# Kernel tuning notes

Measured on AMD Instinct MI355X. Metric: run time of the kernel, lower is better.

The kernel has to match this reference:

```python
import jax, jax.numpy as jnp
import numpy as np

K = 5  # box-blur width along disparity axis

def _blur_disparity(x):
    # depthwise conv1d with ones(K)/K kernel, zero 'same' padding, along axis 1
    N, D, H, W = x.shape
    xp = jnp.pad(x, ((0, 0), (K // 2, K // 2), (0, 0), (0, 0)))
    acc = xp[:, 0:D]
    for s in range(1, K):
        acc = acc + xp[:, s:s + D]
    return acc / K

def _modal_mask(x):
    N, D, H, W = x.shape
    index = jnp.argmax(x, axis=1, keepdims=True)                 # [N,1,H,W] int
    d = jnp.arange(D, dtype=x.dtype).reshape(1, D, 1, 1)
    d2 = jnp.arange(D + 1, dtype=x.dtype).reshape(1, D + 1, 1, 1)
    ones = jnp.ones((N, 1, H, W), dtype=x.dtype)
    x_diff_r = jnp.diff(x, axis=1, prepend=ones, append=ones)    # [N,D+1,H,W]
    x_diff_l = jnp.diff(x, axis=1, prepend=ones)                 # [N,D,H,W]
    # right edge of dominant mode: first positive diff strictly right of peak
    ind_r = ((x_diff_r * (d2 > index)) > 0).astype(jnp.int32)
    index_r = jnp.argmax(ind_r, axis=1, keepdims=True) - 1
    # left edge: last negative diff at/left of peak
    ind_l = ((x_diff_l * (d <= index)) < 0).astype(jnp.int32)
    index_l = D - 1 - jnp.argmax(jnp.flip(ind_l, axis=1), axis=1, keepdims=True)
    mask1 = (d >= index_l) & (d <= index_r)
    r = jnp.minimum(index_r - index, index - index_l)
    mask2 = (d >= index - r) & (d <= index + r)
    valid = jnp.abs(2 * index - index_r - index_l) < 3           # near-symmetric mode
    return jnp.where(valid, mask1, mask2)                        # bool [N,D,H,W]

def setup_inputs() -> dict:
    key = jax.random.key(0)
    N, D, H, W = 2, 192, 256, 512
    x = jax.random.uniform(key, (N, D, H, W), dtype=jnp.float32)
    return {"x": x}

def reference(x) -> jnp.ndarray:
    N, D, H, W = x.shape
    disp = jnp.arange(D, dtype=x.dtype).reshape(1, D, 1, 1)
    x_blur = _blur_disparity(x)
    mask = _modal_mask(x_blur)
    y = x * mask                       # primary mode mass
    z = x - y
    x_blur2 = x_blur * (~mask)
    z = z * _modal_mask(x_blur2)       # secondary mode mass
    valid = (jnp.sum(y, axis=1) >= jnp.sum(z, axis=1)).astype(jnp.float32)[:, None]
    xm = valid * y + (1.0 - valid) * z
    xm = xm / jnp.sum(xm, axis=1, keepdims=True)
    out = jnp.sum(xm * disp, axis=1, keepdims=True)  # [N,1,H,W]
    return out
```

## Files before the change

### kernel.cpp

```cpp
#include <hip/hip_runtime.h>
#include <math.h>

namespace {
constexpr int D     = 192;
constexpr int HW    = 256 * 512;
constexpr int TOTAL = 2 * HW;

__device__ __forceinline__ float div5(float s) {
    const float c = 0.2f;
    float q = s * c;
    float r = __builtin_fmaf(-5.0f, q, s);
    return __builtin_fmaf(r, c, q);
}

struct Machine {
    float bprev, maxv;
    int   index, last_fall, index_l, index_r;
    bool  r_found;

    __device__ __forceinline__ void init() {
        bprev = 1.0f;
        maxv  = -INFINITY;
        index = 0; last_fall = 0; index_l = 0;
        index_r = D - 1;
        r_found = false;
    }

    __device__ __forceinline__ void step(int d, float b) {
        float diff = b - bprev;
        bool fall  = diff < 0.0f;
        last_fall  = fall ? d : last_fall;
        bool am    = b > maxv;
        maxv       = am ? b : maxv;
        index      = am ? d : index;
        index_l    = am ? last_fall : index_l;
        bool rise  = (diff > 0.0f) & (!r_found) & (!am);
        index_r    = am ? (D - 1) : (rise ? (d - 1) : index_r);
        r_found    = am ? false : (r_found | rise);
        bprev      = b;
    }

    __device__ __forceinline__ void finish(int& lo, int& hi) const {
        int r = min(index_r - index, index - index_l);
        int t = 2 * index - index_r - index_l;
        bool valid = (t > -3) && (t < 3);
        lo = valid ? index_l : (index - r);
        hi = valid ? index_r : (index + r);
    }
};

__device__ __forceinline__ bool in_range(int d, int lo, unsigned width) {
    return (unsigned)(d - lo) <= width;
}
}

extern "C" __global__ void __launch_bounds__(256)
dme_kernel(const float* __restrict__ x, float* __restrict__ out)
{
    const int n  = blockIdx.x >> 9;
    const int hw = ((blockIdx.x & 511) << 8) | threadIdx.x;
    const float* __restrict__ col = x + (size_t)n * (size_t)(D * HW) + hw;

    Machine m1; m1.init();
    {
        float w0 = 0.f, w1 = 0.f;
        float w2 = col[0], w3 = col[HW];
        float cur[8], nxt[8];
        #pragma unroll
        for (int j = 0; j < 8; ++j) cur[j] = col[(size_t)(2 + j) * HW];
        int d = 0;
        auto step8 = [&](const float (&L)[8]) {
            #pragma unroll
            for (int j = 0; j < 8; ++j) {
                float s = w0 + w1; s += w2; s += w3; s += L[j];
                m1.step(d, div5(s));
                w0 = w1; w1 = w2; w2 = w3; w3 = L[j]; ++d;
            }
        };
        for (int k = 0; k < 22; ++k) {
            #pragma unroll
            for (int j = 0; j < 8; ++j) nxt[j] = col[(size_t)(8 * k + 10 + j) * HW];
            step8(cur);
            #pragma unroll
            for (int j = 0; j < 8; ++j) cur[j] = nxt[j];
        }
        #pragma unroll
        for (int j = 0; j < 8; ++j)
            nxt[j] = (186 + j < D) ? col[(size_t)(186 + j) * HW] : 0.0f;
        step8(cur);
        #pragma unroll
        for (int j = 0; j < 8; ++j) cur[j] = nxt[j];
        step8(cur);
    }
    int lo1, hi1; m1.finish(lo1, hi1);
    unsigned wd1 = (unsigned)(hi1 - lo1);

    Machine m2; m2.init();
    float sum_y = 0.f, wsum_y = 0.f;
    {
        float w0 = 0.f, w1 = 0.f;
        float w2 = col[0], w3 = col[HW];
        float cur[8], nxt[8];
        #pragma unroll
        for (int j = 0; j < 8; ++j) cur[j] = col[(size_t)(2 + j) * HW];
        int d = 0; float fd = 0.0f;
        auto step8 = [&](const float (&L)[8]) {
            #pragma unroll
            for (int j = 0; j < 8; ++j) {
                float s = w0 + w1; s += w2; s += w3; s += L[j];
                float b = div5(s);
                bool in1 = in_range(d, lo1, wd1);
                m2.step(d, in1 ? 0.0f : b);
                sum_y += in1 ? w2 : 0.f;
                float t = in1 ? fd : 0.f;
                wsum_y = __builtin_fmaf(t, w2, wsum_y);
                w0 = w1; w1 = w2; w2 = w3; w3 = L[j]; ++d; fd += 1.0f;
            }
        };
        for (int k = 0; k < 22; ++k) {
            #pragma unroll
            for (int j = 0; j < 8; ++j) nxt[j] = col[(size_t)(8 * k + 10 + j) * HW];
            step8(cur);
            #pragma unroll
            for (int j = 0; j < 8; ++j) cur[j] = nxt[j];
        }
        #pragma unroll
        for (int j = 0; j < 8; ++j)
            nxt[j] = (186 + j < D) ? col[(size_t)(186 + j) * HW] : 0.0f;
        step8(cur);
        #pragma unroll
        for (int j = 0; j < 8; ++j) cur[j] = nxt[j];
        step8(cur);
    }
    int lo2, hi2; m2.finish(lo2, hi2);
    unsigned wd2 = (unsigned)(hi2 - lo2);

    float sum_z = 0.f, wsum_z = 0.f;
    {
        float cur[8], nxt[8];
        #pragma unroll
        for (int j = 0; j < 8; ++j) cur[j] = col[(size_t)j * HW];
        int d = 0; float fd = 0.0f;
        auto step8 = [&](const float (&L)[8]) {
            #pragma unroll
            for (int j = 0; j < 8; ++j) {
                bool z = in_range(d, lo2, wd2) & !in_range(d, lo1, wd1);
                sum_z += z ? L[j] : 0.f;
                float t = z ? fd : 0.f;
                wsum_z = __builtin_fmaf(t, L[j], wsum_z);
                ++d; fd += 1.0f;
            }
        };
        for (int k = 0; k < 23; ++k) {
            #pragma unroll
            for (int j = 0; j < 8; ++j) nxt[j] = col[(size_t)(8 * k + 8 + j) * HW];
            step8(cur);
            #pragma unroll
            for (int j = 0; j < 8; ++j) cur[j] = nxt[j];
        }
        step8(cur);
    }

    bool  v = (sum_y >= sum_z);
    float S = v ? sum_y  : sum_z;
    float W = v ? wsum_y : wsum_z;
    out[hw + n * HW] = W / S;
}

extern "C" void kernel_launch(void* const* d_in, const int* in_sizes, int n_in,
                              void* d_out, int out_size, void* d_ws, size_t ws_size,
                              hipStream_t stream)
{
    const float* x   = (const float*)d_in[0];
    float*       out = (float*)d_out;
    dim3 block(256), grid(TOTAL / 256);
    hipLaunchKernelGGL(dme_kernel, grid, block, 0, stream, x, out);
}
```

Before: 326.5 us.

## Split disparity scan across two half-waves with associative state merge

Each pixel is now handled by two lanes, each scanning half of the disparity axis (0-95 and 96-191). The modal-mask state machines gain a first_rise field so the halves can be combined through cross-lane shuffles. The final accumulation pass is also divided: lane A sums the primary mode and lane B sums the secondary mode, and the two results are exchanged by shuffle. The aim is to double thread-level parallelism and shorten each thread's serial dependency chain, at the cost of more shuffles, a more involved merge, and twice the grid size. Each lane still reads all 192 slices in the final pass, so global memory traffic is not reduced.

Result: slower. 345.5 us (+5.8%).

```diff
diff --git a/kernel.cpp b/kernel.cpp
--- a/kernel.cpp
+++ b/kernel.cpp
@@ -13,17 +13,20 @@
     return __builtin_fmaf(r, c, q);
 }
 
-struct Machine {
+__device__ __forceinline__ bool in_range(int d, int lo, unsigned width) {
+    return (unsigned)(d - lo) <= width;
+}
+
+struct SegMachine {
     float bprev, maxv;
-    int   index, last_fall, index_l, index_r;
+    int   index, last_fall, index_l, index_r, first_rise;
     bool  r_found;
 
-    __device__ __forceinline__ void init() {
-        bprev = 1.0f;
-        maxv  = -INFINITY;
-        index = 0; last_fall = 0; index_l = 0;
-        index_r = D - 1;
-        r_found = false;
+    __device__ __forceinline__ void init(float bp, bool isB) {
+        bprev = bp; maxv = -INFINITY; index = 0;
+        last_fall = isB ? -1 : 0;
+        index_l   = isB ? -1 : 0;
+        index_r = D - 1; first_rise = -1; r_found = false;
     }
 
     __device__ __forceinline__ void step(int d, float b) {
@@ -31,140 +34,178 @@
         bool fall  = diff < 0.0f;
         last_fall  = fall ? d : last_fall;
         bool am    = b > maxv;
-        maxv       = am ? b : maxv;
+        maxv       = fmaxf(b, maxv);
         index      = am ? d : index;
         index_l    = am ? last_fall : index_l;
-        bool rise  = (diff > 0.0f) & (!r_found) & (!am);
-        index_r    = am ? (D - 1) : (rise ? (d - 1) : index_r);
-        r_found    = am ? false : (r_found | rise);
+        bool rise  = diff > 0.0f;
+        first_rise = (rise && (first_rise < 0)) ? d : first_rise;
+        bool ra    = rise & (!r_found) & (!am);
+        index_r    = am ? (D - 1) : (ra ? (d - 1) : index_r);
+        r_found    = am ? false : (r_found | ra);
         bprev      = b;
     }
-
-    __device__ __forceinline__ void finish(int& lo, int& hi) const {
-        int r = min(index_r - index, index - index_l);
-        int t = 2 * index - index_r - index_l;
-        bool valid = (t > -3) && (t < 3);
-        lo = valid ? index_l : (index - r);
-        hi = valid ? index_r : (index + r);
-    }
 };
 
-__device__ __forceinline__ bool in_range(int d, int lo, unsigned width) {
-    return (unsigned)(d - lo) <= width;
-}
-}
-
-extern "C" __global__ void __launch_bounds__(256)
+__device__ __forceinline__ void merge_bounds(const SegMachine& me, bool isB,
+                                             int& lo, unsigned& wd) {
+    float o_maxv  = __shfl_xor(me.maxv, 32);
+    int o_index   = __shfl_xor(me.index, 32);
+    int o_index_l = __shfl_xor(me.index_l, 32);
+    int o_index_r = __shfl_xor(me.index_r, 32);
+    int o_lf      = __shfl_xor(me.last_fall, 32);
+    int o_fr      = __shfl_xor(me.first_rise, 32);
+    int o_rf      = __shfl_xor((int)me.r_found, 32);
+
+    float Amax = isB ? o_maxv : me.maxv;
+    int  Aidx  = isB ? o_index   : me.index;
+    int  Ail   = isB ? o_index_l : me.index_l;
+    int  Air   = isB ? o_index_r : me.index_r;
+    int  Alf   = isB ? o_lf      : me.last_fall;
+    bool Arf   = isB ? (o_rf != 0) : me.r_found;
+    float Bmax = isB ? me.maxv : o_maxv;
+    int  Bidx  = isB ? me.index   : o_index;
+    int  Bil   = isB ? me.index_l : o_index_l;
+    int  Bir   = isB ? me.index_r : o_index_r;
+    int  Bfr   = isB ? me.first_rise : o_fr;
+
+    bool inA    = Amax >= Bmax;
+    int index   = inA ? Aidx : Bidx;
+    int index_l = inA ? Ail : (Bil >= 0 ? Bil : Alf);
+    int index_r = inA ? (Arf ? Air : (Bfr >= 0 ? Bfr - 1 : D - 1)) : Bir;
+
+    int r = min(index_r - index, index - index_l);
+    int t = 2 * index - index_r - index_l;
+    bool valid = (t > -3) && (t < 3);
+    lo = valid ? index_l : (index - r);
+    int hi = valid ? index_r : (index + r);
+    wd = (unsigned)(hi - lo);
+}
+
+template<typename F>
+__device__ __forceinline__ void stream96(const float* __restrict__ col, int d0,
+                                         float w0, float w1, float w2, float w3,
+                                         F&& f) {
+    float cur[8], nxt[8];
+    #pragma unroll
+    for (int j = 0; j < 8; ++j) cur[j] = col[(size_t)(d0 + 2 + j) * HW];
+    int d = d0;
+    for (int k = 0; k < 11; ++k) {
+        int base = d0 + 10 + 8 * k;
+        if (k < 10) {
+            #pragma unroll
+            for (int j = 0; j < 8; ++j) nxt[j] = col[(size_t)(base + j) * HW];
+        } else {
+            #pragma unroll
+            for (int j = 0; j < 8; ++j) {
+                int idx = base + j;
+                float v = col[(size_t)min(idx, D - 1) * HW];
+                nxt[j] = (idx < D) ? v : 0.0f;
+            }
+        }
+        #pragma unroll
+        for (int j = 0; j < 8; ++j) {
+            float s = w0 + w1; s += w2; s += w3; s += cur[j];
+            f(d, div5(s), w2);
+            w0 = w1; w1 = w2; w2 = w3; w3 = cur[j]; ++d;
+        }
+        #pragma unroll
+        for (int j = 0; j < 8; ++j) cur[j] = nxt[j];
+    }
+    #pragma unroll
+    for (int j = 0; j < 8; ++j) {
+        float s = w0 + w1; s += w2; s += w3; s += cur[j];
+        f(d, div5(s), w2);
+        w0 = w1; w1 = w2; w2 = w3; w3 = cur[j]; ++d;
+    }
+}
+}
+
+extern "C" __global__ void __launch_bounds__(256, 8)
 dme_kernel(const float* __restrict__ x, float* __restrict__ out)
 {
-    const int n  = blockIdx.x >> 9;
-    const int hw = ((blockIdx.x & 511) << 8) | threadIdx.x;
+    const int  lane = threadIdx.x & 63;
+    const int  wv   = threadIdx.x >> 6;
+    const bool isB  = lane >= 32;
+    const int  pix  = blockIdx.x * 128 + wv * 32 + (lane & 31);
+    const int  n    = pix >> 17;
+    const int  hw   = pix & (HW - 1);
     const float* __restrict__ col = x + (size_t)n * (size_t)(D * HW) + hw;
 
-    Machine m1; m1.init();
+    const int d0 = isB ? 96 : 0;
+
+    float t0, t1, t2, t3, t4;
     {
-        float w0 = 0.f, w1 = 0.f;
-        float w2 = col[0], w3 = col[HW];
-        float cur[8], nxt[8];
-        #pragma unroll
-        for (int j = 0; j < 8; ++j) cur[j] = col[(size_t)(2 + j) * HW];
-        int d = 0;
-        auto step8 = [&](const float (&L)[8]) {
-            #pragma unroll
-            for (int j = 0; j < 8; ++j) {
-                float s = w0 + w1; s += w2; s += w3; s += L[j];
-                m1.step(d, div5(s));
-                w0 = w1; w1 = w2; w2 = w3; w3 = L[j]; ++d;
-            }
-        };
-        for (int k = 0; k < 22; ++k) {
-            #pragma unroll
-            for (int j = 0; j < 8; ++j) nxt[j] = col[(size_t)(8 * k + 10 + j) * HW];
-            step8(cur);
-            #pragma unroll
-            for (int j = 0; j < 8; ++j) cur[j] = nxt[j];
-        }
-        #pragma unroll
-        for (int j = 0; j < 8; ++j)
-            nxt[j] = (186 + j < D) ? col[(size_t)(186 + j) * HW] : 0.0f;
-        step8(cur);
-        #pragma unroll
-        for (int j = 0; j < 8; ++j) cur[j] = nxt[j];
-        step8(cur);
-    }
-    int lo1, hi1; m1.finish(lo1, hi1);
-    unsigned wd1 = (unsigned)(hi1 - lo1);
-
-    Machine m2; m2.init();
-    float sum_y = 0.f, wsum_y = 0.f;
-    {
-        float w0 = 0.f, w1 = 0.f;
-        float w2 = col[0], w3 = col[HW];
-        float cur[8], nxt[8];
-        #pragma unroll
-        for (int j = 0; j < 8; ++j) cur[j] = col[(size_t)(2 + j) * HW];
-        int d = 0; float fd = 0.0f;
-        auto step8 = [&](const float (&L)[8]) {
-            #pragma unroll
-            for (int j = 0; j < 8; ++j) {
-                float s = w0 + w1; s += w2; s += w3; s += L[j];
-                float b = div5(s);
-                bool in1 = in_range(d, lo1, wd1);
-                m2.step(d, in1 ? 0.0f : b);
-                sum_y += in1 ? w2 : 0.f;
-                float t = in1 ? fd : 0.f;
-                wsum_y = __builtin_fmaf(t, w2, wsum_y);
-                w0 = w1; w1 = w2; w2 = w3; w3 = L[j]; ++d; fd += 1.0f;
-            }
-        };
-        for (int k = 0; k < 22; ++k) {
-            #pragma unroll
-            for (int j = 0; j < 8; ++j) nxt[j] = col[(size_t)(8 * k + 10 + j) * HW];
-            step8(cur);
-            #pragma unroll
-            for (int j = 0; j < 8; ++j) cur[j] = nxt[j];
-        }
-        #pragma unroll
-        for (int j = 0; j < 8; ++j)
-            nxt[j] = (186 + j < D) ? col[(size_t)(186 + j) * HW] : 0.0f;
-        step8(cur);
-        #pragma unroll
-        for (int j = 0; j < 8; ++j) cur[j] = nxt[j];
-        step8(cur);
-    }
-    int lo2, hi2; m2.finish(lo2, hi2);
-    unsigned wd2 = (unsigned)(hi2 - lo2);
-
-    float sum_z = 0.f, wsum_z = 0.f;
+        int b0 = isB ? 93 : 0;
+        t0 = col[(size_t)(b0 + 0) * HW];
+        t1 = col[(size_t)(b0 + 1) * HW];
+        t2 = col[(size_t)(b0 + 2) * HW];
+        t3 = col[(size_t)(b0 + 3) * HW];
+        t4 = col[(size_t)(b0 + 4) * HW];
+    }
+    float s95 = t0 + t1; s95 += t2; s95 += t3; s95 += t4;
+    s95 = div5(s95);
+    const float w0i = isB ? t1 : 0.f;
+    const float w1i = isB ? t2 : 0.f;
+    const float w2i = isB ? t3 : t0;
+    const float w3i = isB ? t4 : t1;
+
+    SegMachine m1; m1.init(isB ? s95 : 1.0f, isB);
+    stream96(col, d0, w0i, w1i, w2i, w3i,
+             [&](int d, float b, float) { m1.step(d, b); });
+    int lo1; unsigned wd1;
+    merge_bounds(m1, isB, lo1, wd1);
+
+    float bp2 = isB ? (in_range(95, lo1, wd1) ? 0.0f : s95) : 1.0f;
+    SegMachine m2; m2.init(bp2, isB);
+    stream96(col, d0, w0i, w1i, w2i, w3i,
+             [&](int d, float b, float) {
+                 m2.step(d, in_range(d, lo1, wd1) ? 0.0f : b);
+             });
+    int lo2; unsigned wd2;
+    merge_bounds(m2, isB, lo2, wd2);
+
+    float sum = 0.f, wsum = 0.f, fd = 0.f;
+    const int loS = isB ? lo2 : lo1;
+    const unsigned wdS = isB ? wd2 : wd1;
     {
         float cur[8], nxt[8];
         #pragma unroll
         for (int j = 0; j < 8; ++j) cur[j] = col[(size_t)j * HW];
-        int d = 0; float fd = 0.0f;
-        auto step8 = [&](const float (&L)[8]) {
+        int d = 0;
+        for (int k = 0; k < 23; ++k) {
+            #pragma unroll
+            for (int j = 0; j < 8; ++j) nxt[j] = col[(size_t)(8 * k + 8 + j) * HW];
             #pragma unroll
             for (int j = 0; j < 8; ++j) {
-                bool z = in_range(d, lo2, wd2) & !in_range(d, lo1, wd1);
-                sum_z += z ? L[j] : 0.f;
-                float t = z ? fd : 0.f;
-                wsum_z = __builtin_fmaf(t, L[j], wsum_z);
+                bool inS = in_range(d, loS, wdS);
+                bool use = isB ? (inS & !in_range(d, lo1, wd1)) : inS;
+                float term = use ? cur[j] : 0.f;
+                sum += term;
+                wsum = __builtin_fmaf(fd, term, wsum);
                 ++d; fd += 1.0f;
             }
-        };
-        for (int k = 0; k < 23; ++k) {
-            #pragma unroll
-            for (int j = 0; j < 8; ++j) nxt[j] = col[(size_t)(8 * k + 8 + j) * HW];
-            step8(cur);
             #pragma unroll
             for (int j = 0; j < 8; ++j) cur[j] = nxt[j];
         }
-        step8(cur);
-    }
-
-    bool  v = (sum_y >= sum_z);
-    float S = v ? sum_y  : sum_z;
-    float W = v ? wsum_y : wsum_z;
-    out[hw + n * HW] = W / S;
+        #pragma unroll
+        for (int j = 0; j < 8; ++j) {
+            bool inS = in_range(d, loS, wdS);
+            bool use = isB ? (inS & !in_range(d, lo1, wd1)) : inS;
+            float term = use ? cur[j] : 0.f;
+            sum += term;
+            wsum = __builtin_fmaf(fd, term, wsum);
+            ++d; fd += 1.0f;
+        }
+    }
+
+    float o_sum  = __shfl_xor(sum, 32);
+    float o_wsum = __shfl_xor(wsum, 32);
+    if (!isB) {
+        bool  v = (sum >= o_sum);
+        float Ssel = v ? sum  : o_sum;
+        float Wsel = v ? wsum : o_wsum;
+        out[pix] = Wsel / Ssel;
+    }
 }
 
 extern "C" void kernel_launch(void* const* d_in, const int* in_sizes, int n_in,
@@ -173,6 +214,6 @@
 {
     const float* x   = (const float*)d_in[0];
     float*       out = (float*)d_out;
-    dim3 block(256), grid(TOTAL / 256);
+    dim3 block(256), grid(TOTAL / 128);
     hipLaunchKernelGGL(dme_kernel, grid, block, 0, stream, x, out);
 }
```
